# Performance work log

Hardware: AMD Instinct MI355X
Metric: run time of the kernel (lower is better)

The kernel has to match this reference:

```python
import jax, jax.numpy as jnp
import numpy as np

D_MODEL = 1024
N_HEADS = 16
HEAD_DIM = D_MODEL // N_HEADS


def setup_inputs() -> dict:
    key = jax.random.key(0)
    k1, k2, k3 = jax.random.split(key, 3)
    x = jax.random.normal(k1, (4, 2048, D_MODEL), dtype=jnp.float32)
    # nn.Linear(d_model, 3*d_model, bias=False): weight [3*d_model, d_model]
    w_qkv = jax.random.normal(k2, (3 * D_MODEL, D_MODEL), dtype=jnp.float32) / np.sqrt(D_MODEL)
    w_out = jax.random.normal(k3, (D_MODEL, D_MODEL), dtype=jnp.float32) / np.sqrt(D_MODEL)
    return {"x": x, "w_qkv": w_qkv, "w_out": w_out}


def reference(x, w_qkv, w_out):
    B, T, C = x.shape
    qkv = jnp.einsum('btc,fc->btf', x, w_qkv)  # [B,T,3C]
    q, k, v = jnp.split(qkv, 3, axis=-1)

    def heads(t):
        return t.reshape(B, T, N_HEADS, HEAD_DIM).transpose(0, 2, 1, 3)  # [B,H,T,D]

    q, k, v = heads(q), heads(k), heads(v)
    scale = 1.0 / np.sqrt(HEAD_DIM).astype(np.float32)
    attn = jnp.einsum('bhqd,bhkd->bhqk', q, k) * scale  # [B,H,T,T]
    causal = jnp.tril(jnp.ones((T, T), dtype=bool))
    attn = jnp.where(causal[None, None], attn, -jnp.inf)
    attn = jax.nn.softmax(attn, axis=-1)
    out = jnp.einsum('bhqk,bhkd->bhqd', attn, v)
    out = out.transpose(0, 2, 1, 3).reshape(B, T, C)
    return jnp.einsum('btc,fc->btf', out, w_out)
```

## Files before the change

### kernel.cpp

```cpp
#include <hip/hip_runtime.h>
#include <hip/hip_bf16.h>
#include <type_traits>


typedef __attribute__((ext_vector_type(8))) short bf16x8;
typedef __attribute__((ext_vector_type(4))) float f32x4;

#define LDS_AS(p) ((__attribute__((address_space(3))) void*)(p))
#define GLB_AS(p) ((const __attribute__((address_space(1))) void*)(p))

__global__ __launch_bounds__(256) void cvt_f32_bf16(const float* __restrict__ in,
                                                    __hip_bfloat16* __restrict__ out,
                                                    int n4) {
  int i = blockIdx.x * 256 + threadIdx.x;
  if (i >= n4) return;
  float4 v = reinterpret_cast<const float4*>(in)[i];
  __hip_bfloat16 b0 = __float2bfloat16(v.x);
  __hip_bfloat16 b1 = __float2bfloat16(v.y);
  __hip_bfloat16 b2 = __float2bfloat16(v.z);
  __hip_bfloat16 b3 = __float2bfloat16(v.w);
  ushort4 u;
  u.x = *reinterpret_cast<unsigned short*>(&b0);
  u.y = *reinterpret_cast<unsigned short*>(&b1);
  u.z = *reinterpret_cast<unsigned short*>(&b2);
  u.w = *reinterpret_cast<unsigned short*>(&b3);
  reinterpret_cast<ushort4*>(out)[i] = u;
}

template <typename TOUT>
__global__ __launch_bounds__(256) void gemm_bt(const __hip_bfloat16* __restrict__ A,
                                               const __hip_bfloat16* __restrict__ B,
                                               TOUT* __restrict__ C,
                                               int M, int N, int K) {
  __shared__ __hip_bfloat16 As[128 * 64];
  __shared__ __hip_bfloat16 Bs[128 * 64];
  const int tid = threadIdx.x;
  const int lane = tid & 63;
  const int wid = tid >> 6;
  const int l15 = lane & 15, l4 = lane >> 4;
  const int m0 = blockIdx.x * 128, n0 = blockIdx.y * 128;
  const int wr = (wid >> 1) * 64;
  const int wc = (wid & 1) * 64;
  f32x4 acc[4][4] = {};

  for (int kt = 0; kt < K; kt += 64) {
#pragma unroll
    for (int i = 0; i < 4; ++i) {
      const int slot = i * 256 + tid;
      const int row = slot >> 3, c8 = slot & 7;
      __builtin_amdgcn_global_load_lds(GLB_AS(A + (size_t)(m0 + row) * K + kt + c8 * 8),
                                       LDS_AS((char*)As + slot * 16), 16, 0, 0);
      __builtin_amdgcn_global_load_lds(GLB_AS(B + (size_t)(n0 + row) * K + kt + c8 * 8),
                                       LDS_AS((char*)Bs + slot * 16), 16, 0, 0);
    }
    __syncthreads();
#pragma unroll
    for (int kk = 0; kk < 2; ++kk) {
      bf16x8 af[4], bfr[4];
#pragma unroll
      for (int mi = 0; mi < 4; ++mi)
        af[mi] = *reinterpret_cast<const bf16x8*>(As + (wr + mi * 16 + l15) * 64 + kk * 32 + l4 * 8);
#pragma unroll
      for (int ni = 0; ni < 4; ++ni)
        bfr[ni] = *reinterpret_cast<const bf16x8*>(Bs + (wc + ni * 16 + l15) * 64 + kk * 32 + l4 * 8);
#pragma unroll
      for (int mi = 0; mi < 4; ++mi)
#pragma unroll
        for (int ni = 0; ni < 4; ++ni)
          acc[mi][ni] = __builtin_amdgcn_mfma_f32_16x16x32_bf16(af[mi], bfr[ni], acc[mi][ni], 0, 0, 0);
    }
    __syncthreads();
  }
#pragma unroll
  for (int mi = 0; mi < 4; ++mi)
#pragma unroll
    for (int ni = 0; ni < 4; ++ni)
#pragma unroll
      for (int j = 0; j < 4; ++j) {
        const int m = m0 + wr + mi * 16 + l4 * 4 + j;
        const int n = n0 + wc + ni * 16 + l15;
        if constexpr (std::is_same<TOUT, float>::value)
          C[(size_t)m * N + n] = acc[mi][ni][j];
        else
          C[(size_t)m * N + n] = __float2bfloat16(acc[mi][ni][j]);
      }
}

__global__ __launch_bounds__(512, 2) void attn_causal(const __hip_bfloat16* __restrict__ qkv,
                                                      __hip_bfloat16* __restrict__ o) {
  constexpr int T = 2048, F = 3072, C = 1024;
  __shared__ __hip_bfloat16 Ks[64 * 72];
  __shared__ __hip_bfloat16 Vts[64 * 72];
  __shared__ __hip_bfloat16 Ps[8][16 * 72];
  const int tid = threadIdx.x;
  const int wid = tid >> 6, lane = tid & 63;
  const int l15 = lane & 15, l4 = lane >> 4;
  const int x = blockIdx.x, h = blockIdx.y, b = blockIdx.z;
  const int qt = (wid < 4) ? x : (7 - x);
  const int nt = 4 * (7 - x) + 4;
  const int tmax = 4 * qt + (wid & 3);
  const int hoff = h * 64;
  const __hip_bfloat16* base = qkv + (size_t)b * T * F;
  const int Q0 = qt * 256 + (wid & 3) * 64;

  constexpr float SC = 0.125f * 1.44269504088896f;

  bf16x8 aq[4][2];
#pragma unroll
  for (int f = 0; f < 4; ++f)
#pragma unroll
    for (int kk = 0; kk < 2; ++kk)
      aq[f][kk] = *reinterpret_cast<const bf16x8*>(base + (size_t)(Q0 + f * 16 + l15) * F + hoff + kk * 32 + l4 * 8);

  f32x4 acc[4][4] = {};
  float mrun[4], lrun[4];
#pragma unroll
  for (int f = 0; f < 4; ++f) { mrun[f] = -1e30f; lrun[f] = 0.f; }

  const int sV = tid;
  const int sK = tid - 256;
  bf16x8 sreg0, sreg1;
  if (wid < 4) {
    const size_t vr = (size_t)(2 * (sV >> 3)) * F + hoff + 2 * C + (sV & 7) * 8;
    sreg0 = *reinterpret_cast<const bf16x8*>(base + vr);
    sreg1 = *reinterpret_cast<const bf16x8*>(base + vr + F);
  } else {
    sreg0 = *reinterpret_cast<const bf16x8*>(base + (size_t)(sK >> 3) * F + hoff + C + (sK & 7) * 8);
    sreg1 = *reinterpret_cast<const bf16x8*>(base + (size_t)(32 + (sK >> 3)) * F + hoff + C + (sK & 7) * 8);
  }

  for (int t = 0; t < nt; ++t) {
    unsigned pkr[8];
    if (wid < 4) {
      const unsigned short* a0 = reinterpret_cast<const unsigned short*>(&sreg0);
      const unsigned short* a1 = reinterpret_cast<const unsigned short*>(&sreg1);
      const int c8 = sV & 7;
      unsigned pk[8], tw[8];
#pragma unroll
      for (int j = 0; j < 8; ++j) pk[j] = (unsigned)a0[j] | ((unsigned)a1[j] << 16);
#pragma unroll
      for (int j = 0; j < 8; ++j) tw[j] = (c8 & 4) ? pk[(j + 4) & 7] : pk[j];
#pragma unroll
      for (int j = 0; j < 8; ++j) pkr[j] = (c8 & 2) ? tw[(j + 2) & 7] : tw[j];
#pragma unroll
      for (int j = 0; j < 8; ++j) tw[j] = (c8 & 1) ? pkr[(j + 1) & 7] : pkr[j];
#pragma unroll
      for (int j = 0; j < 8; ++j) pkr[j] = tw[j];
    }
    __syncthreads();
    if (wid < 4) {
      const int r2 = sV >> 3, c8 = sV & 7;
#pragma unroll
      for (int jj = 0; jj < 8; ++jj) {
        const int d = c8 * 8 + ((jj + c8) & 7);
        *reinterpret_cast<unsigned*>(&Vts[d * 72 + 2 * r2]) = pkr[jj];
      }
    } else {
      *reinterpret_cast<bf16x8*>(&Ks[(sK >> 3) * 72 + (sK & 7) * 8]) = sreg0;
      *reinterpret_cast<bf16x8*>(&Ks[(32 + (sK >> 3)) * 72 + (sK & 7) * 8]) = sreg1;
    }
    __syncthreads();
    if (t + 1 < nt) {
      const int kn = (t + 1) * 64;
      if (wid < 4) {
        const size_t vr = (size_t)(kn + 2 * (sV >> 3)) * F + hoff + 2 * C + (sV & 7) * 8;
        sreg0 = *reinterpret_cast<const bf16x8*>(base + vr);
        sreg1 = *reinterpret_cast<const bf16x8*>(base + vr + F);
      } else {
        sreg0 = *reinterpret_cast<const bf16x8*>(base + (size_t)(kn + (sK >> 3)) * F + hoff + C + (sK & 7) * 8);
        sreg1 = *reinterpret_cast<const bf16x8*>(base + (size_t)(kn + 32 + (sK >> 3)) * F + hoff + C + (sK & 7) * 8);
      }
    }
    if (t > tmax) continue;
    const bool diag = (t == tmax);

    bf16x8 kf[4][2], vf[4][2];
#pragma unroll
    for (int kt = 0; kt < 4; ++kt)
#pragma unroll
      for (int kk = 0; kk < 2; ++kk)
        kf[kt][kk] = *reinterpret_cast<const bf16x8*>(Ks + (kt * 16 + l15) * 72 + kk * 32 + l4 * 8);
#pragma unroll
    for (int di = 0; di < 4; ++di)
#pragma unroll
      for (int kk = 0; kk < 2; ++kk)
        vf[di][kk] = *reinterpret_cast<const bf16x8*>(Vts + (di * 16 + l15) * 72 + kk * 32 + l4 * 8);

    __hip_bfloat16* pw = Ps[wid];
#pragma unroll
    for (int f = 0; f < 4; ++f) {
      f32x4 s[4];
#pragma unroll
      for (int kt = 0; kt < 4; ++kt) {
        f32x4 z = {};
        z = __builtin_amdgcn_mfma_f32_16x16x32_bf16(kf[kt][0], aq[f][0], z, 0, 0, 0);
        z = __builtin_amdgcn_mfma_f32_16x16x32_bf16(kf[kt][1], aq[f][1], z, 0, 0, 0);
        s[kt] = z;
      }

      if (diag) {
        const int ql = f * 16 + l15;
#pragma unroll
        for (int kt = 0; kt < 4; ++kt)
#pragma unroll
          for (int j = 0; j < 4; ++j) {
            const int kvl = kt * 16 + l4 * 4 + j;
            s[kt][j] = (kvl <= ql) ? s[kt][j] * SC : -1e30f;
          }
      } else {
#pragma unroll
        for (int kt = 0; kt < 4; ++kt)
#pragma unroll
          for (int j = 0; j < 4; ++j) s[kt][j] *= SC;
      }

      float mt = -1e30f;
#pragma unroll
      for (int kt = 0; kt < 4; ++kt)
        mt = fmaxf(mt, fmaxf(fmaxf(s[kt][0], s[kt][1]), fmaxf(s[kt][2], s[kt][3])));
      mt = fmaxf(mt, __shfl_xor(mt, 16, 64));
      mt = fmaxf(mt, __shfl_xor(mt, 32, 64));
      const float mnew = fmaxf(mrun[f], mt);
      const float sco = exp2f(mrun[f] - mnew);
      float rs = 0.f;
#pragma unroll
      for (int kt = 0; kt < 4; ++kt) {
        float p0 = exp2f(s[kt][0] - mnew), p1 = exp2f(s[kt][1] - mnew);
        float p2 = exp2f(s[kt][2] - mnew), p3 = exp2f(s[kt][3] - mnew);
        s[kt][0] = p0; s[kt][1] = p1; s[kt][2] = p2; s[kt][3] = p3;
        rs += (p0 + p1) + (p2 + p3);
      }
      rs += __shfl_xor(rs, 16, 64);
      rs += __shfl_xor(rs, 32, 64);
      lrun[f] = lrun[f] * sco + rs;
      mrun[f] = mnew;
#pragma unroll
      for (int di = 0; di < 4; ++di) acc[f][di] *= sco;

#pragma unroll
      for (int kt = 0; kt < 4; ++kt) {
        __hip_bfloat16 e0 = __float2bfloat16(s[kt][0]);
        __hip_bfloat16 e1 = __float2bfloat16(s[kt][1]);
        __hip_bfloat16 e2 = __float2bfloat16(s[kt][2]);
        __hip_bfloat16 e3 = __float2bfloat16(s[kt][3]);
        unsigned w0 = (unsigned)*reinterpret_cast<unsigned short*>(&e0) |
                      ((unsigned)*reinterpret_cast<unsigned short*>(&e1) << 16);
        unsigned w1 = (unsigned)*reinterpret_cast<unsigned short*>(&e2) |
                      ((unsigned)*reinterpret_cast<unsigned short*>(&e3) << 16);
        unsigned long long dw = (unsigned long long)w0 | ((unsigned long long)w1 << 32);
        *reinterpret_cast<unsigned long long*>(&pw[l15 * 72 + kt * 16 + l4 * 4]) = dw;
      }
      asm volatile("s_waitcnt lgkmcnt(0)" ::: "memory");
      bf16x8 pa0 = *reinterpret_cast<const bf16x8*>(pw + l15 * 72 + l4 * 8);
      bf16x8 pa1 = *reinterpret_cast<const bf16x8*>(pw + l15 * 72 + 32 + l4 * 8);

#pragma unroll
      for (int di = 0; di < 4; ++di) {
        acc[f][di] = __builtin_amdgcn_mfma_f32_16x16x32_bf16(vf[di][0], pa0, acc[f][di], 0, 0, 0);
        acc[f][di] = __builtin_amdgcn_mfma_f32_16x16x32_bf16(vf[di][1], pa1, acc[f][di], 0, 0, 0);
      }
    }
  }

#pragma unroll
  for (int f = 0; f < 4; ++f) {
    const float inv = 1.0f / lrun[f];
    __hip_bfloat16* op = o + (size_t)((size_t)b * T + Q0 + f * 16 + l15) * C + hoff;
#pragma unroll
    for (int di = 0; di < 4; ++di) {
      ushort4 u;
      __hip_bfloat16 e0 = __float2bfloat16(acc[f][di][0] * inv);
      __hip_bfloat16 e1 = __float2bfloat16(acc[f][di][1] * inv);
      __hip_bfloat16 e2 = __float2bfloat16(acc[f][di][2] * inv);
      __hip_bfloat16 e3 = __float2bfloat16(acc[f][di][3] * inv);
      u.x = *reinterpret_cast<unsigned short*>(&e0);
      u.y = *reinterpret_cast<unsigned short*>(&e1);
      u.z = *reinterpret_cast<unsigned short*>(&e2);
      u.w = *reinterpret_cast<unsigned short*>(&e3);
      *reinterpret_cast<ushort4*>(op + di * 16 + l4 * 4) = u;
    }
  }
}

extern "C" void kernel_launch(void* const* d_in, const int* in_sizes, int n_in,
                              void* d_out, int out_size, void* d_ws, size_t ws_size,
                              hipStream_t stream) {
  const float* x = (const float*)d_in[0];
  const float* w_qkv = (const float*)d_in[1];
  const float* w_out = (const float*)d_in[2];
  float* out = (float*)d_out;

  constexpr int B = 4, T = 2048, C = 1024, F = 3 * C;
  constexpr int M = B * T;

  __hip_bfloat16* xb = (__hip_bfloat16*)d_ws;
  __hip_bfloat16* wqkvb = xb + (size_t)M * C;
  __hip_bfloat16* woutb = wqkvb + (size_t)F * C;
  __hip_bfloat16* qkvb = woutb + (size_t)C * C;
  __hip_bfloat16* attnb = qkvb + (size_t)M * F;

  cvt_f32_bf16<<<(M * C / 4 + 255) / 256, 256, 0, stream>>>(x, xb, M * C / 4);
  cvt_f32_bf16<<<(F * C / 4 + 255) / 256, 256, 0, stream>>>(w_qkv, wqkvb, F * C / 4);
  cvt_f32_bf16<<<(C * C / 4 + 255) / 256, 256, 0, stream>>>(w_out, woutb, C * C / 4);

  gemm_bt<__hip_bfloat16><<<dim3(M / 128, F / 128), 256, 0, stream>>>(xb, wqkvb, qkvb, M, F, C);

  attn_causal<<<dim3(4, 16, B), 512, 0, stream>>>(qkvb, attnb);

  gemm_bt<float><<<dim3(M / 128, C / 128), 256, 0, stream>>>(attnb, woutb, out, M, C, C);
}
```

Baseline: 244.8 us.

## Double-buffer K/V tiles, prescale Q, defer softmax rescale, use packed bf16 convert

Double-buffers the K and V shared-memory tiles, which removes one __syncthreads per KV tile. Q is pre-multiplied by the softmax scale at load time, so the per-score multiply goes away. The online-softmax rescale of the accumulator is skipped when the new row max stays within 8 of the running max, and the row-max reduction is reorganised into a tree. The fp32-to-bf16 packing uses v_cvt_pk_bf16_f32 inline asm. In exchange the kernel uses more LDS, rounds Q once more to bf16 after scaling, and risks exp2 values up to 2^8 in P, which affects precision.

```diff
diff --git a/kernel.cpp b/kernel.cpp
--- a/kernel.cpp
+++ b/kernel.cpp
@@ -89,8 +89,8 @@
 __global__ __launch_bounds__(512, 2) void attn_causal(const __hip_bfloat16* __restrict__ qkv,
                                                       __hip_bfloat16* __restrict__ o) {
   constexpr int T = 2048, F = 3072, C = 1024;
-  __shared__ __hip_bfloat16 Ks[64 * 72];
-  __shared__ __hip_bfloat16 Vts[64 * 72];
+  __shared__ __hip_bfloat16 Ks[2][64 * 72];
+  __shared__ __hip_bfloat16 Vts[2][64 * 72];
   __shared__ __hip_bfloat16 Ps[8][16 * 72];
   const int tid = threadIdx.x;
   const int wid = tid >> 6, lane = tid & 63;
@@ -109,8 +109,17 @@
 #pragma unroll
   for (int f = 0; f < 4; ++f)
 #pragma unroll
-    for (int kk = 0; kk < 2; ++kk)
-      aq[f][kk] = *reinterpret_cast<const bf16x8*>(base + (size_t)(Q0 + f * 16 + l15) * F + hoff + kk * 32 + l4 * 8);
+    for (int kk = 0; kk < 2; ++kk) {
+      bf16x8 q = *reinterpret_cast<const bf16x8*>(base + (size_t)(Q0 + f * 16 + l15) * F + hoff + kk * 32 + l4 * 8);
+#pragma unroll
+      for (int e = 0; e < 8; ++e) {
+        const unsigned short raw = (unsigned short)q[e];
+        const float fv = __uint_as_float((unsigned)raw << 16) * SC;
+        __hip_bfloat16 qs = __float2bfloat16(fv);
+        q[e] = *reinterpret_cast<short*>(&qs);
+      }
+      aq[f][kk] = q;
+    }
 
   f32x4 acc[4][4] = {};
   float mrun[4], lrun[4];
@@ -130,12 +139,12 @@
   }
 
   for (int t = 0; t < nt; ++t) {
-    unsigned pkr[8];
+    const int cur = t & 1;
     if (wid < 4) {
       const unsigned short* a0 = reinterpret_cast<const unsigned short*>(&sreg0);
       const unsigned short* a1 = reinterpret_cast<const unsigned short*>(&sreg1);
-      const int c8 = sV & 7;
-      unsigned pk[8], tw[8];
+      const int c8 = sV & 7, r2 = sV >> 3;
+      unsigned pk[8], tw[8], pkr[8];
 #pragma unroll
       for (int j = 0; j < 8; ++j) pk[j] = (unsigned)a0[j] | ((unsigned)a1[j] << 16);
 #pragma unroll
@@ -144,20 +153,14 @@
       for (int j = 0; j < 8; ++j) pkr[j] = (c8 & 2) ? tw[(j + 2) & 7] : tw[j];
 #pragma unroll
       for (int j = 0; j < 8; ++j) tw[j] = (c8 & 1) ? pkr[(j + 1) & 7] : pkr[j];
-#pragma unroll
-      for (int j = 0; j < 8; ++j) pkr[j] = tw[j];
-    }
-    __syncthreads();
-    if (wid < 4) {
-      const int r2 = sV >> 3, c8 = sV & 7;
 #pragma unroll
       for (int jj = 0; jj < 8; ++jj) {
         const int d = c8 * 8 + ((jj + c8) & 7);
-        *reinterpret_cast<unsigned*>(&Vts[d * 72 + 2 * r2]) = pkr[jj];
+        *reinterpret_cast<unsigned*>(&Vts[cur][d * 72 + 2 * r2]) = tw[jj];
       }
     } else {
-      *reinterpret_cast<bf16x8*>(&Ks[(sK >> 3) * 72 + (sK & 7) * 8]) = sreg0;
-      *reinterpret_cast<bf16x8*>(&Ks[(32 + (sK >> 3)) * 72 + (sK & 7) * 8]) = sreg1;
+      *reinterpret_cast<bf16x8*>(&Ks[cur][(sK >> 3) * 72 + (sK & 7) * 8]) = sreg0;
+      *reinterpret_cast<bf16x8*>(&Ks[cur][(32 + (sK >> 3)) * 72 + (sK & 7) * 8]) = sreg1;
     }
     __syncthreads();
     if (t + 1 < nt) {
@@ -179,12 +182,12 @@
     for (int kt = 0; kt < 4; ++kt)
 #pragma unroll
       for (int kk = 0; kk < 2; ++kk)
-        kf[kt][kk] = *reinterpret_cast<const bf16x8*>(Ks + (kt * 16 + l15) * 72 + kk * 32 + l4 * 8);
+        kf[kt][kk] = *reinterpret_cast<const bf16x8*>(&Ks[cur][(kt * 16 + l15) * 72 + kk * 32 + l4 * 8]);
 #pragma unroll
     for (int di = 0; di < 4; ++di)
 #pragma unroll
       for (int kk = 0; kk < 2; ++kk)
-        vf[di][kk] = *reinterpret_cast<const bf16x8*>(Vts + (di * 16 + l15) * 72 + kk * 32 + l4 * 8);
+        vf[di][kk] = *reinterpret_cast<const bf16x8*>(&Vts[cur][(di * 16 + l15) * 72 + kk * 32 + l4 * 8]);
 
     __hip_bfloat16* pw = Ps[wid];
 #pragma unroll
@@ -197,7 +200,6 @@
         z = __builtin_amdgcn_mfma_f32_16x16x32_bf16(kf[kt][1], aq[f][1], z, 0, 0, 0);
         s[kt] = z;
       }
-
       if (diag) {
         const int ql = f * 16 + l15;
 #pragma unroll
@@ -205,23 +207,20 @@
 #pragma unroll
           for (int j = 0; j < 4; ++j) {
             const int kvl = kt * 16 + l4 * 4 + j;
-            s[kt][j] = (kvl <= ql) ? s[kt][j] * SC : -1e30f;
+            s[kt][j] = (kvl <= ql) ? s[kt][j] : -1e30f;
           }
-      } else {
-#pragma unroll
-        for (int kt = 0; kt < 4; ++kt)
-#pragma unroll
-          for (int j = 0; j < 4; ++j) s[kt][j] *= SC;
-      }
-
-      float mt = -1e30f;
-#pragma unroll
-      for (int kt = 0; kt < 4; ++kt)
-        mt = fmaxf(mt, fmaxf(fmaxf(s[kt][0], s[kt][1]), fmaxf(s[kt][2], s[kt][3])));
+      }
+
+      float t0 = fmaxf(fmaxf(s[0][0], s[0][1]), s[0][2]);
+      float t1 = fmaxf(fmaxf(s[0][3], s[1][0]), s[1][1]);
+      float t2 = fmaxf(fmaxf(s[1][2], s[1][3]), s[2][0]);
+      float t3 = fmaxf(fmaxf(s[2][1], s[2][2]), s[2][3]);
+      float t4 = fmaxf(fmaxf(s[3][0], s[3][1]), s[3][2]);
+      float mt = fmaxf(fmaxf(fmaxf(t0, t1), fmaxf(t2, t3)), fmaxf(t4, s[3][3]));
       mt = fmaxf(mt, __shfl_xor(mt, 16, 64));
       mt = fmaxf(mt, __shfl_xor(mt, 32, 64));
-      const float mnew = fmaxf(mrun[f], mt);
-      const float sco = exp2f(mrun[f] - mnew);
+      const bool defer = __all(mt <= mrun[f] + 8.f);
+      const float mnew = defer ? mrun[f] : fmaxf(mrun[f], mt);
       float rs = 0.f;
 #pragma unroll
       for (int kt = 0; kt < 4; ++kt) {
@@ -232,21 +231,21 @@
       }
       rs += __shfl_xor(rs, 16, 64);
       rs += __shfl_xor(rs, 32, 64);
-      lrun[f] = lrun[f] * sco + rs;
-      mrun[f] = mnew;
-#pragma unroll
-      for (int di = 0; di < 4; ++di) acc[f][di] *= sco;
+      if (defer) {
+        lrun[f] += rs;
+      } else {
+        const float sco = exp2f(mrun[f] - mnew);
+        lrun[f] = lrun[f] * sco + rs;
+        mrun[f] = mnew;
+#pragma unroll
+        for (int di = 0; di < 4; ++di) acc[f][di] *= sco;
+      }
 
 #pragma unroll
       for (int kt = 0; kt < 4; ++kt) {
-        __hip_bfloat16 e0 = __float2bfloat16(s[kt][0]);
-        __hip_bfloat16 e1 = __float2bfloat16(s[kt][1]);
-        __hip_bfloat16 e2 = __float2bfloat16(s[kt][2]);
-        __hip_bfloat16 e3 = __float2bfloat16(s[kt][3]);
-        unsigned w0 = (unsigned)*reinterpret_cast<unsigned short*>(&e0) |
-                      ((unsigned)*reinterpret_cast<unsigned short*>(&e1) << 16);
-        unsigned w1 = (unsigned)*reinterpret_cast<unsigned short*>(&e2) |
-                      ((unsigned)*reinterpret_cast<unsigned short*>(&e3) << 16);
+        unsigned w0, w1;
+        asm("v_cvt_pk_bf16_f32 %0, %1, %2" : "=v"(w0) : "v"(s[kt][0]), "v"(s[kt][1]));
+        asm("v_cvt_pk_bf16_f32 %0, %1, %2" : "=v"(w1) : "v"(s[kt][2]), "v"(s[kt][3]));
         unsigned long long dw = (unsigned long long)w0 | ((unsigned long long)w1 << 32);
         *reinterpret_cast<unsigned long long*>(&pw[l15 * 72 + kt * 16 + l4 * 4]) = dw;
       }
```

Measured after the change: 231.1 us. 5.6% less time.
